# Performance work log

Measured on AMD Instinct MI355X. Metric: run time of the kernel, lower is better.

The kernel has to match this reference:

```python
import jax, jax.numpy as jnp
import numpy as np

N_HEADS = 16
ROPE_BASE = 10000.0

def _rope_cos_sin(seq_len, head_dim):
    # freqs[t, j] = t / base**(2j/head_dim), j over head_dim//2 pairs
    inv_freq = 1.0 / (ROPE_BASE ** (jnp.arange(0, head_dim, 2, dtype=jnp.float32) / head_dim))
    t = jnp.arange(seq_len, dtype=jnp.float32)
    freqs = t[:, None] * inv_freq[None, :]          # [S, hd/2]
    return jnp.cos(freqs), jnp.sin(freqs)

def _apply_rope(x, cos, sin):
    # x: [B, S, H, hd]; pairs are interleaved (even, odd) -> complex (re, im)
    xr = x[..., 0::2]
    xi = x[..., 1::2]
    c = cos[None, :, None, :]
    s = sin[None, :, None, :]
    out_r = xr * c - xi * s
    out_i = xr * s + xi * c
    # interleave back: [..., hd/2, 2] -> [..., hd]
    return jnp.stack([out_r, out_i], axis=-1).reshape(x.shape)

def setup_inputs() -> dict:
    key = jax.random.key(0)
    ks = jax.random.split(key, 5)
    B, S, D = 2, 2048, 2048
    x = jax.random.normal(ks[0], (B, S, D), dtype=jnp.float32)
    w_scale = 0.02
    wq = jax.random.normal(ks[1], (D, D), dtype=jnp.float32) * w_scale
    wk = jax.random.normal(ks[2], (D, D), dtype=jnp.float32) * w_scale
    wv = jax.random.normal(ks[3], (D, D), dtype=jnp.float32) * w_scale
    wo = jax.random.normal(ks[4], (D, D), dtype=jnp.float32) * w_scale
    return {"x": x, "wq": wq, "wk": wk, "wv": wv, "wo": wo}

def reference(x, wq, wk, wv, wo):
    B, S, D = x.shape
    H = N_HEADS
    hd = D // H
    # QKV projections (torch Linear: y = x @ W^T)
    q = (x @ wq.T).reshape(B, S, H, hd)
    k = (x @ wk.T).reshape(B, S, H, hd)
    v = (x @ wv.T).reshape(B, S, H, hd)
    cos, sin = _rope_cos_sin(S, hd)
    q = _apply_rope(q, cos, sin)
    k = _apply_rope(k, cos, sin)
    # -> [B, H, S, hd]
    q = q.transpose(0, 2, 1, 3)
    k = k.transpose(0, 2, 1, 3)
    v = v.transpose(0, 2, 1, 3)
    scale = 1.0 / jnp.sqrt(jnp.float32(hd))
    scores = jnp.einsum('bhqd,bhkd->bhqk', q, k) * scale
    causal = jnp.tril(jnp.ones((S, S), dtype=bool))
    scores = jnp.where(causal[None, None], scores, jnp.float32(-1e30))
    probs = jax.nn.softmax(scores, axis=-1)
    attn = jnp.einsum('bhqk,bhkd->bhqd', probs, v)  # [B, H, S, hd]
    attn = attn.transpose(0, 2, 1, 3).reshape(B, S, D)
    return attn @ wo.T
```

## Files before the change

### kernel.cpp

```cpp
#include <hip/hip_runtime.h>
#include <hip/hip_bf16.h>

using bf16 = __hip_bfloat16;
typedef __attribute__((ext_vector_type(8))) short short8;
typedef __attribute__((ext_vector_type(4))) float floatx4;
typedef __attribute__((ext_vector_type(2))) float floatx2;

#define GLDS16(g, l)                                                        \
  __builtin_amdgcn_global_load_lds(                                         \
      (const __attribute__((address_space(1))) void*)(g),                   \
      (__attribute__((address_space(3))) void*)(l), 16, 0, 0)

#define MFMA16(a, b, c) __builtin_amdgcn_mfma_f32_16x16x32_bf16(a, b, c, 0, 0, 0)

__device__ __forceinline__ short f2b(float x) {
  union { bf16 h; short s; } u;
  u.h = __float2bfloat16(x);
  return u.s;
}
__device__ __forceinline__ void st(float* p, float v) { *p = v; }
__device__ __forceinline__ void st(bf16* p, float v) { *p = __float2bfloat16(v); }

template <int CTRL>
__device__ __forceinline__ float dpp_f(float x) {
  return __int_as_float(__builtin_amdgcn_update_dpp(
      0, __float_as_int(x), CTRL, 0xF, 0xF, true));
}
__device__ __forceinline__ float red16_max(float x) {
  x = fmaxf(x, dpp_f<0xB1>(x));
  x = fmaxf(x, dpp_f<0x4E>(x));
  x = fmaxf(x, dpp_f<0x141>(x));
  x = fmaxf(x, dpp_f<0x140>(x));
  return x;
}
__device__ __forceinline__ float red16_sum(float x) {
  x += dpp_f<0xB1>(x);
  x += dpp_f<0x4E>(x);
  x += dpp_f<0x141>(x);
  x += dpp_f<0x140>(x);
  return x;
}

__global__ void cast_kernel(const float* __restrict__ in, bf16* __restrict__ out,
                            long n) {
  long i = ((long)blockIdx.x * blockDim.x + threadIdx.x) * 8;
  if (i >= n) return;
  floatx4 a = *(const floatx4*)(in + i);
  floatx4 b = *(const floatx4*)(in + i + 4);
  short8 r;
  r[0] = f2b(a[0]); r[1] = f2b(a[1]); r[2] = f2b(a[2]); r[3] = f2b(a[3]);
  r[4] = f2b(b[0]); r[5] = f2b(b[1]); r[6] = f2b(b[2]); r[7] = f2b(b[3]);
  *(short8*)(out + i) = r;
}

__global__ void rope_tab_kernel(floatx2* __restrict__ tab) {
  const int t = blockIdx.x * blockDim.x + threadIdx.x;
  const int s = t >> 6, p = t & 63;
  const float invf = exp2f(-(float)p * (13.287712379549449f / 64.0f));
  float sn, cs;
  sincosf((float)s * invf, &sn, &cs);
  floatx2 e; e[0] = cs; e[1] = sn;
  tab[t] = e;
}

__device__ __forceinline__ void gemm_core(
    const bf16* __restrict__ A, const bf16* __restrict__ B, int K,
    long m0, long n0, bf16* As, bf16* Bs, floatx4 (&acc)[8][4])
{
  const int tid  = threadIdx.x;
  const int wave = tid >> 6;
  const int lane = tid & 63;
  const int quad = lane >> 4;
  const int l16  = lane & 15;
  const int wr = wave >> 1;
  const int wc = wave & 1;

  long ga[4];
  int aoff[4];
#pragma unroll
  for (int i = 0; i < 4; i++) {
    const int c = i * 256 + tid;
    const int row = c >> 2;
    const int gch = (c & 3) ^ ((c >> 3) & 3);
    ga[i] = (m0 + row) * (long)K + gch * 8;
    aoff[i] = (i * 256 + wave * 64) * 8;
  }
  long gb[2];
  int boff[2];
#pragma unroll
  for (int i = 0; i < 2; i++) {
    const int c = i * 256 + tid;
    const int row = c >> 2;
    const int gch = (c & 3) ^ ((c >> 3) & 3);
    gb[i] = (n0 + row) * (long)K + gch * 8;
    boff[i] = (i * 256 + wave * 64) * 8;
  }

  const int qs = (quad ^ ((l16 >> 1) & 3)) * 8;

#pragma unroll
  for (int mi = 0; mi < 8; mi++)
#pragma unroll
    for (int ni = 0; ni < 4; ni++) {
      floatx4 z = {0.f, 0.f, 0.f, 0.f};
      acc[mi][ni] = z;
    }

  const int NT = K >> 5;

#pragma unroll
  for (int t = 0; t < 2; t++) {
    bf16* Ad = As + t * 8192;
    bf16* Bd = Bs + t * 4096;
    const long kk = (long)t * 32;
#pragma unroll
    for (int i = 0; i < 4; i++) GLDS16(A + ga[i] + kk, Ad + aoff[i]);
#pragma unroll
    for (int i = 0; i < 2; i++) GLDS16(B + gb[i] + kk, Bd + boff[i]);
  }

  int sl = 0;
  for (int t = 0; t < NT; t++) {
    if (t < NT - 1) asm volatile("s_waitcnt vmcnt(6)" ::: "memory");
    else            asm volatile("s_waitcnt vmcnt(0)" ::: "memory");
    __builtin_amdgcn_s_barrier();

    const bf16* Ab = As + sl * 8192;
    const bf16* Bb = Bs + sl * 4096;

    short8 a[8], b[4];
#pragma unroll
    for (int mi = 0; mi < 8; mi++)
      a[mi] = *(const short8*)(Ab + (wr * 128 + mi * 16 + l16) * 32 + qs);
#pragma unroll
    for (int ni = 0; ni < 4; ni++)
      b[ni] = *(const short8*)(Bb + (wc * 64 + ni * 16 + l16) * 32 + qs);

    if (t + 2 < NT) {
      int s2 = sl + 2; if (s2 >= 3) s2 -= 3;
      bf16* Ad = As + s2 * 8192;
      bf16* Bd = Bs + s2 * 4096;
      const long kk = (long)(t + 2) * 32;
#pragma unroll
      for (int i = 0; i < 4; i++) GLDS16(A + ga[i] + kk, Ad + aoff[i]);
#pragma unroll
      for (int i = 0; i < 2; i++) GLDS16(B + gb[i] + kk, Bd + boff[i]);
    }

    asm volatile("s_waitcnt lgkmcnt(0)" ::: "memory");
    __builtin_amdgcn_sched_barrier(0);
    __builtin_amdgcn_s_setprio(1);
#pragma unroll
    for (int mi = 0; mi < 8; mi++)
#pragma unroll
      for (int ni = 0; ni < 4; ni++)
        acc[mi][ni] = MFMA16(a[mi], b[ni], acc[mi][ni]);
    __builtin_amdgcn_s_setprio(0);

    sl++; if (sl >= 3) sl = 0;
  }
}

__global__ __launch_bounds__(256, 2) void qkv_gemm(
    const bf16* __restrict__ A,
    const bf16* __restrict__ B0, const bf16* __restrict__ B1,
    const bf16* __restrict__ B2,
    bf16* __restrict__ C0, bf16* __restrict__ C1, bf16* __restrict__ Cvt,
    const floatx2* __restrict__ rtab,
    int M, int N, int K)
{
  __shared__ __align__(16) bf16 As[3 * 8192];
  __shared__ __align__(16) bf16 Bs[3 * 4096];

  const int sel = blockIdx.y >> 4;
  const long m0 = (long)blockIdx.x * 256;
  const long n0 = (long)(blockIdx.y & 15) * 128;
  const bf16* B = (sel == 0) ? B0 : ((sel == 1) ? B1 : B2);

  floatx4 acc[8][4];
  gemm_core(A, B, K, m0, n0, As, Bs, acc);

  const int tid  = threadIdx.x;
  const int wave = tid >> 6;
  const int lane = tid & 63;
  const int quad = lane >> 4;
  const int l16  = lane & 15;
  const int wr = wave >> 1;
  const int wc = wave & 1;

  if (sel < 2) {
    bf16* C = (sel == 0) ? C0 : C1;
    const float qscale = (sel == 0)
        ? (0.08838834764831845f * 1.4426950408889634f) : 1.0f;
    const float sgn = (l16 & 1) ? 1.0f : -1.0f;
#pragma unroll
    for (int ni = 0; ni < 4; ni++) {
      const int n = (int)n0 + wc * 64 + ni * 16 + l16;
      const int p = (n & 127) >> 1;
#pragma unroll
      for (int mi = 0; mi < 8; mi++) {
        floatx4 v = acc[mi][ni];
        const int mbase = (int)m0 + wr * 128 + mi * 16 + quad * 4;
#pragma unroll
        for (int r = 0; r < 4; r++) {
          const int spos = (mbase + r) & 2047;
          const floatx2 cssn = rtab[spos * 64 + p];
          const float pv = dpp_f<0xB1>(v[r]);
          const float outv = (v[r] * cssn[0] + pv * (sgn * cssn[1])) * qscale;
          st(&C[(long)(mbase + r) * N + n], outv);
        }
      }
    }
  } else {
#pragma unroll
    for (int ni = 0; ni < 4; ni++) {
      const int n = (int)n0 + wc * 64 + ni * 16 + l16;
      const int hh = n >> 7, d = n & 127;
#pragma unroll
      for (int mi = 0; mi < 8; mi++) {
        floatx4 v = acc[mi][ni];
        const int m = (int)m0 + wr * 128 + mi * 16 + quad * 4;
        const int bb = m >> 11, s = m & 2047;
        unsigned long long pk =
            (unsigned long long)(unsigned short)f2b(v[0]) |
            ((unsigned long long)(unsigned short)f2b(v[1]) << 16) |
            ((unsigned long long)(unsigned short)f2b(v[2]) << 32) |
            ((unsigned long long)(unsigned short)f2b(v[3]) << 48);
        *(unsigned long long*)(Cvt + ((long)((bb * 16 + hh) * 128 + d)) * 2048 + s) = pk;
      }
    }
  }
}

__global__ __launch_bounds__(256, 2) void gemm_out(
    const bf16* __restrict__ A, const bf16* __restrict__ B,
    float* __restrict__ C, int M, int N, int K)
{
  __shared__ __align__(16) bf16 As[3 * 8192];
  __shared__ __align__(16) bf16 Bs[3 * 4096];
  const long m0 = (long)blockIdx.x * 256;
  const long n0 = (long)blockIdx.y * 128;

  floatx4 acc[8][4];
  gemm_core(A, B, K, m0, n0, As, Bs, acc);

  const int tid  = threadIdx.x;
  const int wave = tid >> 6;
  const int lane = tid & 63;
  const int quad = lane >> 4;
  const int l16  = lane & 15;
  const int wr = wave >> 1;
  const int wc = wave & 1;

#pragma unroll
  for (int mi = 0; mi < 8; mi++)
#pragma unroll
    for (int ni = 0; ni < 4; ni++) {
      floatx4 v = acc[mi][ni];
      const long row = m0 + wr * 128 + mi * 16 + quad * 4;
      const long col = n0 + wc * 64 + ni * 16 + l16;
#pragma unroll
      for (int r = 0; r < 4; r++)
        C[(row + r) * (long)N + col] = v[r];
    }
}

#define NEG_BIG (-30000.0f)

__global__ __launch_bounds__(256) void flash_attn(
    const bf16* __restrict__ q, const bf16* __restrict__ k,
    const bf16* __restrict__ vt, bf16* __restrict__ o, int S)
{
  __shared__ bf16 Ks[64 * 136];
  __shared__ bf16 Vt[128 * 72];
  __shared__ bf16 Ps[4][32 * 72];

  const int tid  = threadIdx.x;
  const int wave = tid >> 6;
  const int lane = tid & 63;
  const int quad = lane >> 4;
  const int l16  = lane & 15;

  const int bh = blockIdx.x;
  const int b  = bh >> 4, h = bh & 15;
  const int q0 = ((int)gridDim.y - 1 - (int)blockIdx.y) * 128;

  const bf16* Qb = q + ((long)b * S * 16 + h) * 128;
  const bf16* Kb = k + ((long)b * S * 16 + h) * 128;
  const bf16* Vg = vt + (long)bh * 128 * S;
  bf16*       Ob = o + ((long)b * S * 16 + h) * 128;

  int kr[4], kc[4], vr[4], vc[4];
#pragma unroll
  for (int it = 0; it < 4; it++) {
    const int c = tid + it * 256;
    kr[it] = c >> 4;  kc[it] = (c & 15) * 8;
    vr[it] = c >> 3;  vc[it] = (c & 7) * 8;
  }

  short8 aq[2][4];
#pragma unroll
  for (int mi = 0; mi < 2; mi++)
#pragma unroll
    for (int kt = 0; kt < 4; kt++)
      aq[mi][kt] = *(const short8*)(
          Qb + (long)(q0 + wave * 32 + mi * 16 + l16) * 2048 + kt * 32 + quad * 8);

  float m_i[2][4], l_i[2][4];
  floatx4 oacc[2][8];
  const floatx4 zero4 = {0.f, 0.f, 0.f, 0.f};
#pragma unroll
  for (int mi = 0; mi < 2; mi++) {
#pragma unroll
    for (int r = 0; r < 4; r++) { m_i[mi][r] = NEG_BIG; l_i[mi][r] = 0.f; }
#pragma unroll
    for (int dt = 0; dt < 8; dt++) oacc[mi][dt] = zero4;
  }

  const int wrow0 = q0 + wave * 32;
  const int last  = q0 + 64;

  short8 kreg[4], vreg[4];
#pragma unroll
  for (int it = 0; it < 4; it++) {
    kreg[it] = *(const short8*)(Kb + (long)kr[it] * 2048 + kc[it]);
    vreg[it] = *(const short8*)(Vg + (long)vr[it] * S + vc[it]);
  }

  for (int kt0 = 0; kt0 <= last; kt0 += 64) {
    __syncthreads();

#pragma unroll
    for (int it = 0; it < 4; it++) {
      *(short8*)(Ks + kr[it] * 136 + kc[it]) = kreg[it];
      *(short8*)(Vt + vr[it] * 72 + vc[it]) = vreg[it];
    }
    __syncthreads();

    if (kt0 < last) {
      const int n0 = kt0 + 64;
#pragma unroll
      for (int it = 0; it < 4; it++) {
        kreg[it] = *(const short8*)(Kb + (long)(n0 + kr[it]) * 2048 + kc[it]);
        vreg[it] = *(const short8*)(Vg + (long)vr[it] * S + n0 + vc[it]);
      }
    }

    if (kt0 <= wrow0 + 31) {
      floatx4 sc[2][4];
#pragma unroll
      for (int mi = 0; mi < 2; mi++)
#pragma unroll
        for (int nt = 0; nt < 4; nt++) sc[mi][nt] = zero4;

      __builtin_amdgcn_s_setprio(1);
#pragma unroll
      for (int nt = 0; nt < 4; nt++)
#pragma unroll
        for (int kt = 0; kt < 4; kt++) {
          short8 bk = *(const short8*)(Ks + (nt * 16 + l16) * 136 + kt * 32 + quad * 8);
          sc[0][nt] = __builtin_amdgcn_mfma_f32_16x16x32_bf16(aq[0][kt], bk, sc[0][nt], 0, 0, 0);
          sc[1][nt] = __builtin_amdgcn_mfma_f32_16x16x32_bf16(aq[1][kt], bk, sc[1][nt], 0, 0, 0);
        }
      __builtin_amdgcn_s_setprio(0);

      const bool needmask = (kt0 + 63 > wrow0);
      float mx[2][4];
      int allskip = 1;
#pragma unroll
      for (int mi = 0; mi < 2; mi++) {
#pragma unroll
        for (int r = 0; r < 4; r++) {
          const int qr = wrow0 + mi * 16 + quad * 4 + r;
          float m = NEG_BIG;
          if (needmask) {
#pragma unroll
            for (int nt = 0; nt < 4; nt++) {
              const int kc2 = kt0 + nt * 16 + l16;
              float vsc = (kc2 <= qr) ? sc[mi][nt][r] : NEG_BIG;
              sc[mi][nt][r] = vsc;
              m = fmaxf(m, vsc);
            }
          } else {
#pragma unroll
            for (int nt = 0; nt < 4; nt++) m = fmaxf(m, sc[mi][nt][r]);
          }
          m = red16_max(m);
          mx[mi][r] = m;
          allskip &= (m <= m_i[mi][r] + 8.0f) ? 1 : 0;
        }
      }

      if (!__all(allskip)) {
#pragma unroll
        for (int mi = 0; mi < 2; mi++) {
#pragma unroll
          for (int r = 0; r < 4; r++) {
            const float mnew = fmaxf(m_i[mi][r], mx[mi][r]);
            const float alpha = exp2f(m_i[mi][r] - mnew);
            m_i[mi][r] = mnew;
            l_i[mi][r] *= alpha;
#pragma unroll
            for (int dt = 0; dt < 8; dt++) oacc[mi][dt][r] *= alpha;
          }
        }
      }

#pragma unroll
      for (int mi = 0; mi < 2; mi++) {
#pragma unroll
        for (int r = 0; r < 4; r++) {
          float rs = 0.f;
#pragma unroll
          for (int nt = 0; nt < 4; nt++) {
            float p = exp2f(sc[mi][nt][r] - m_i[mi][r]);
            sc[mi][nt][r] = p;
            rs += p;
          }
          rs = red16_sum(rs);
          l_i[mi][r] += rs;
        }
      }

#pragma unroll
      for (int mi = 0; mi < 2; mi++)
#pragma unroll
        for (int nt = 0; nt < 4; nt++)
#pragma unroll
          for (int r = 0; r < 4; r++)
            Ps[wave][(mi * 16 + quad * 4 + r) * 72 + nt * 16 + l16] =
                __float2bfloat16(sc[mi][nt][r]);

      __builtin_amdgcn_s_setprio(1);
#pragma unroll
      for (int ks = 0; ks < 2; ks++) {
        short8 ap0 = *(const short8*)(&Ps[wave][(l16) * 72 + ks * 32 + quad * 8]);
        short8 ap1 = *(const short8*)(&Ps[wave][(16 + l16) * 72 + ks * 32 + quad * 8]);
#pragma unroll
        for (int dt = 0; dt < 8; dt++) {
          short8 bv = *(const short8*)(Vt + (dt * 16 + l16) * 72 + ks * 32 + quad * 8);
          oacc[0][dt] = __builtin_amdgcn_mfma_f32_16x16x32_bf16(ap0, bv, oacc[0][dt], 0, 0, 0);
          oacc[1][dt] = __builtin_amdgcn_mfma_f32_16x16x32_bf16(ap1, bv, oacc[1][dt], 0, 0, 0);
        }
      }
      __builtin_amdgcn_s_setprio(0);
    }
  }

#pragma unroll
  for (int mi = 0; mi < 2; mi++)
#pragma unroll
    for (int r = 0; r < 4; r++) {
      const float inv = 1.0f / l_i[mi][r];
      const long s = q0 + wave * 32 + mi * 16 + quad * 4 + r;
#pragma unroll
      for (int dt = 0; dt < 8; dt++)
        Ob[s * 2048 + dt * 16 + l16] = __float2bfloat16(oacc[mi][dt][r] * inv);
    }
}

extern "C" void kernel_launch(void* const* d_in, const int* in_sizes, int n_in,
                              void* d_out, int out_size, void* d_ws, size_t ws_size,
                              hipStream_t stream) {
  const float* x  = (const float*)d_in[0];
  const float* wq = (const float*)d_in[1];
  const float* wk = (const float*)d_in[2];
  const float* wv = (const float*)d_in[3];
  const float* wo = (const float*)d_in[4];
  float* out = (float*)d_out;

  const int B = 2, S = 2048, D = 2048, H = 16;
  const int M = B * S;
  const long tsz = (long)M * D;
  const long wsz = (long)D * D;

  if (ws_size < 4 * (size_t)tsz * sizeof(bf16)) return;

  bf16* qb  = (bf16*)d_ws;
  bf16* kb  = qb + tsz;
  bf16* vtb = kb + tsz;
  bf16* ab  = vtb + tsz;

  bf16* xb  = (bf16*)d_out;
  bf16* wqb = xb + tsz;
  bf16* wkb = wqb + wsz;
  bf16* wvb = ab;
  floatx2* rtab = (floatx2*)(ab + wsz);
  bf16* wob = qb;

  cast_kernel<<<(int)(tsz / 8 / 256), 256, 0, stream>>>(x,  xb,  tsz);
  cast_kernel<<<(int)(wsz / 8 / 256), 256, 0, stream>>>(wq, wqb, wsz);
  cast_kernel<<<(int)(wsz / 8 / 256), 256, 0, stream>>>(wk, wkb, wsz);
  cast_kernel<<<(int)(wsz / 8 / 256), 256, 0, stream>>>(wv, wvb, wsz);
  rope_tab_kernel<<<(S * 64) / 256, 256, 0, stream>>>(rtab);

  qkv_gemm<<<dim3(16, 48), 256, 0, stream>>>(
      xb, wqb, wkb, wvb, qb, kb, vtb, rtab, M, D, D);

  flash_attn<<<dim3(B * H, S / 128), 256, 0, stream>>>(qb, kb, vtb, ab, S);

  cast_kernel<<<(int)(wsz / 8 / 256), 256, 0, stream>>>(wo, wob, wsz);
  gemm_out<<<dim3(16, 16), 256, 0, stream>>>(ab, wob, out, M, D, D);
}
```

Baseline: 417.3 us.

## Rewrite QKV GEMM as 256x256 tile, 8-wave, phase-interleaved LDS pipeline

The QKV projection GEMM moves from 256x128 tiles with 4 waves and a 3-stage ring to 256x256 tiles with 8 waves and double-buffered LDS. The K loop is split into four barrier-separated phases per tile, and each phase interleaves global-to-LDS loads of later tiles with MFMA quadrants. The goal is more operand reuse per tile and better overlap of loads with compute, in the style of a ping-pong schedule. In exchange the kernel uses 128KB of LDS per block, which limits occupancy, launches half as many blocks, and adds many barriers. The epilogue may also need its wave mapping adjusted for the new 4x2 wave layout.

```diff
diff --git a/kernel.cpp b/kernel.cpp
--- a/kernel.cpp
+++ b/kernel.cpp
@@ -161,7 +161,7 @@
   }
 }
 
-__global__ __launch_bounds__(256, 2) void qkv_gemm(
+__global__ __launch_bounds__(512, 2) void qkv_gemm(
     const bf16* __restrict__ A,
     const bf16* __restrict__ B0, const bf16* __restrict__ B1,
     const bf16* __restrict__ B2,
@@ -169,24 +169,131 @@
     const floatx2* __restrict__ rtab,
     int M, int N, int K)
 {
-  __shared__ __align__(16) bf16 As[3 * 8192];
-  __shared__ __align__(16) bf16 Bs[3 * 4096];
-
-  const int sel = blockIdx.y >> 4;
+  __shared__ __align__(16) bf16 As[32768];
+  __shared__ __align__(16) bf16 Bs[32768];
+
+  const int sel = blockIdx.y >> 3;
   const long m0 = (long)blockIdx.x * 256;
-  const long n0 = (long)(blockIdx.y & 15) * 128;
-  const bf16* B = (sel == 0) ? B0 : ((sel == 1) ? B1 : B2);
-
-  floatx4 acc[8][4];
-  gemm_core(A, B, K, m0, n0, As, Bs, acc);
+  const long n0 = (long)(blockIdx.y & 7) * 256;
+  const bf16* Bw = (sel == 0) ? B0 : ((sel == 1) ? B1 : B2);
 
   const int tid  = threadIdx.x;
   const int wave = tid >> 6;
   const int lane = tid & 63;
   const int quad = lane >> 4;
   const int l16  = lane & 15;
-  const int wr = wave >> 1;
-  const int wc = wave & 1;
+  const int wr = wave >> 2;
+  const int wc = wave & 3;
+
+  long ga0, ga1, gb0, gb1;
+  int lo0, lo1;
+  {
+    const int c0 = tid,       r0 = c0 >> 3, g0 = (c0 & 7) ^ (r0 & 7);
+    const int c1 = 512 + tid, r1 = c1 >> 3, g1 = (c1 & 7) ^ (r1 & 7);
+    ga0 = (m0 + r0) * (long)K + g0 * 8;  lo0 = c0 * 8;
+    ga1 = (m0 + r1) * (long)K + g1 * 8;  lo1 = c1 * 8;
+    gb0 = (n0 + r0) * (long)K + g0 * 8;
+    gb1 = (n0 + r1) * (long)K + g1 * 8;
+  }
+  const long HK = 128 * (long)K;
+  const int NT = K >> 6;
+  const int NI = NT >> 1;
+
+  const int axor = l16 & 7;
+  const int cof0 = ((0 + quad) ^ axor) * 8;
+  const int cof1 = ((4 + quad) ^ axor) * 8;
+  const int abase = wr * 8192 + l16 * 64;
+  const int bbase = (wc >> 1) * 8192 + ((wc & 1) * 64 + l16) * 64;
+
+  bf16* Ae = As;  bf16* Ao = As + 16384;
+  bf16* Be = Bs;  bf16* Bo = Bs + 16384;
+
+  floatx4 acc[8][4];
+#pragma unroll
+  for (int mi = 0; mi < 8; mi++)
+#pragma unroll
+    for (int ni = 0; ni < 4; ni++) {
+      floatx4 z = {0.f, 0.f, 0.f, 0.f};
+      acc[mi][ni] = z;
+    }
+
+#define STG_A(t, h) do { if ((t) < NT) {                                    \
+    bf16* d_ = As + (((t) & 1) << 14) + ((h) << 13);                        \
+    const long s_ = ((long)(t) << 6) + ((h) ? HK : 0);                      \
+    GLDS16(A + ga0 + s_, d_ + lo0);                                         \
+    GLDS16(A + ga1 + s_, d_ + lo1); } } while (0)
+#define STG_B(t, h) do { if ((t) < NT) {                                    \
+    bf16* d_ = Bs + (((t) & 1) << 14) + ((h) << 13);                        \
+    const long s_ = ((long)(t) << 6) + ((h) ? HK : 0);                      \
+    GLDS16(Bw + gb0 + s_, d_ + lo0);                                        \
+    GLDS16(Bw + gb1 + s_, d_ + lo1); } } while (0)
+#define RD_A(Ab, HI) do { _Pragma("unroll")                                 \
+  for (int mf_ = 0; mf_ < 4; mf_++) {                                       \
+    a[mf_][0] = *(const short8*)((Ab) + abase + (HI) + mf_ * 1024 + cof0);  \
+    a[mf_][1] = *(const short8*)((Ab) + abase + (HI) + mf_ * 1024 + cof1);  \
+  } } while (0)
+#define RD_B(Bb, NH, dst) do { _Pragma("unroll")                            \
+  for (int nf_ = 0; nf_ < 2; nf_++) {                                       \
+    dst[nf_][0] = *(const short8*)((Bb) + bbase + (NH) + nf_ * 1024 + cof0);\
+    dst[nf_][1] = *(const short8*)((Bb) + bbase + (NH) + nf_ * 1024 + cof1);\
+  } } while (0)
+#define QMM(MB, NB, bv) do { _Pragma("unroll")                              \
+  for (int mf_ = 0; mf_ < 4; mf_++) { _Pragma("unroll")                     \
+  for (int nf_ = 0; nf_ < 2; nf_++) {                                       \
+    acc[(MB)+mf_][(NB)+nf_] =                                               \
+        MFMA16(a[mf_][0], bv[nf_][0], acc[(MB)+mf_][(NB)+nf_]);             \
+    acc[(MB)+mf_][(NB)+nf_] =                                               \
+        MFMA16(a[mf_][1], bv[nf_][1], acc[(MB)+mf_][(NB)+nf_]);             \
+  } } } while (0)
+#define PH_IN() do {                                                        \
+    __builtin_amdgcn_s_barrier();                                           \
+    asm volatile("s_waitcnt lgkmcnt(0)" ::: "memory");                      \
+    __builtin_amdgcn_sched_barrier(0);                                      \
+    __builtin_amdgcn_s_setprio(1); } while (0)
+#define PH_OUT() do {                                                       \
+    __builtin_amdgcn_s_setprio(0);                                          \
+    __builtin_amdgcn_s_barrier(); } while (0)
+#define PH_OUT_VM(cond) do {                                                \
+    __builtin_amdgcn_s_setprio(0);                                          \
+    if (cond) asm volatile("s_waitcnt vmcnt(4)" ::: "memory");              \
+    else      asm volatile("s_waitcnt vmcnt(0)" ::: "memory");              \
+    __builtin_amdgcn_s_barrier(); } while (0)
+
+  STG_A(0, 0); STG_A(0, 1); STG_B(0, 0); STG_B(0, 1); STG_B(1, 0); STG_B(1, 1);
+  asm volatile("s_waitcnt vmcnt(4)" ::: "memory");
+  __builtin_amdgcn_s_barrier();
+
+  for (int it = 0; it < NI; ++it) {
+    const int t0 = it * 2, t1 = t0 + 1;
+    short8 a[4][2], bA[2][2], bB[2][2];
+
+    RD_A(Ae, 0);  RD_B(Be, 0, bA);  STG_A(t1, 0);
+    PH_IN();  QMM(0, 0, bA);  PH_OUT();
+    RD_B(Be, 2048, bB);             STG_A(t1, 1);
+    PH_IN();  QMM(0, 2, bB);  PH_OUT();
+    RD_A(Ae, 4096);                 STG_B(t0 + 2, 0);
+    PH_IN();  QMM(4, 2, bB);  PH_OUT();
+                                    STG_B(t0 + 2, 1);
+    PH_IN();  QMM(4, 0, bA);  PH_OUT_VM(t0 + 2 < NT);
+
+    RD_A(Ao, 0);  RD_B(Bo, 0, bA);  STG_A(t0 + 2, 0);
+    PH_IN();  QMM(0, 0, bA);  PH_OUT();
+    RD_B(Bo, 2048, bB);             STG_A(t0 + 2, 1);
+    PH_IN();  QMM(0, 2, bB);  PH_OUT();
+    RD_A(Ao, 4096);                 STG_B(t1 + 2, 0);
+    PH_IN();  QMM(4, 2, bB);  PH_OUT();
+                                    STG_B(t1 + 2, 1);
+    PH_IN();  QMM(4, 0, bA);  PH_OUT_VM(t1 + 2 < NT);
+  }
+
+#undef STG_A
+#undef STG_B
+#undef RD_A
+#undef RD_B
+#undef QMM
+#undef PH_IN
+#undef PH_OUT
+#undef PH_OUT_VM
 
   if (sel < 2) {
     bf16* C = (sel == 0) ? C0 : C1;
@@ -494,7 +601,7 @@
   cast_kernel<<<(int)(wsz / 8 / 256), 256, 0, stream>>>(wv, wvb, wsz);
   rope_tab_kernel<<<(S * 64) / 256, 256, 0, stream>>>(rtab);
 
-  qkv_gemm<<<dim3(16, 48), 256, 0, stream>>>(
+  qkv_gemm<<<dim3(16, 24), 512, 0, stream>>>(
       xb, wqb, wkb, wvb, qb, kb, vtb, rtab, M, D, D);
 
   flash_attn<<<dim3(B * H, S / 128), 256, 0, stream>>>(qb, kb, vtb, ab, S);
```

Result: slower. 428.5 us (+2.7%).
